# Kernel optimization log

Measured on AMD Instinct MI355X. Metric: run time of the kernel, lower is better.

## Reference

```python
import jax, jax.numpy as jnp
import numpy as np

NUM_CLASSES = 81
THRESHOLD = 0.5
NEGPOS_RATIO = 3
VARIANCE = (0.1, 0.2)


def point_form(p):
    # center-size -> corner form
    return jnp.concatenate([p[:, :2] - p[:, 2:] / 2, p[:, :2] + p[:, 2:] / 2], axis=1)


def jaccard(box_a, box_b):
    # box_a: [O,4] corners, box_b: [P,4] corners -> IoU [O,P]
    lt = jnp.maximum(box_a[:, None, :2], box_b[None, :, :2])
    rb = jnp.minimum(box_a[:, None, 2:], box_b[None, :, 2:])
    wh = jnp.clip(rb - lt, 0.0)
    inter = wh[..., 0] * wh[..., 1]
    area_a = ((box_a[:, 2] - box_a[:, 0]) * (box_a[:, 3] - box_a[:, 1]))[:, None]
    area_b = ((box_b[:, 2] - box_b[:, 0]) * (box_b[:, 3] - box_b[:, 1]))[None, :]
    return inter / (area_a + area_b - inter)


def encode(matched, priors, variances):
    # matched: [P,4] corner GT, priors: [P,4] center-size
    g_cxcy = (matched[:, :2] + matched[:, 2:]) / 2 - priors[:, :2]
    g_cxcy = g_cxcy / (variances[0] * priors[:, 2:])
    g_wh = (matched[:, 2:] - matched[:, :2]) / priors[:, 2:]
    g_wh = jnp.log(g_wh) / variances[1]
    return jnp.concatenate([g_cxcy, g_wh], axis=1)


def match_one(truths, labels, priors):
    overlaps = jaccard(truths, point_form(priors))   # [O,P]
    best_prior_idx = jnp.argmax(overlaps, axis=1)     # [O] best prior per truth
    best_truth_overlap = jnp.max(overlaps, axis=0)    # [P]
    best_truth_idx = jnp.argmax(overlaps, axis=0)     # [P] best truth per prior
    # force each truth's best prior to match that truth
    best_truth_overlap = best_truth_overlap.at[best_prior_idx].set(2.0)
    best_truth_idx = best_truth_idx.at[best_prior_idx].set(jnp.arange(truths.shape[0]))
    matched = truths[best_truth_idx]                  # [P,4]
    conf = labels[best_truth_idx].astype(jnp.int32) + 1
    conf = jnp.where(best_truth_overlap < THRESHOLD, 0, conf)
    loc = encode(matched, priors, VARIANCE)
    return loc, conf


def _loss(loc_data, conf_data, targets, priors):
    B, P, C = conf_data.shape
    loc_t, conf_t = jax.vmap(lambda t: match_one(t[:, :4], t[:, 4], priors))(targets)
    pos = conf_t > 0                                  # [B,P]
    # smooth-L1 (beta=1) over positive priors, sum reduction
    d = loc_data - loc_t
    sl1 = jnp.where(jnp.abs(d) < 1.0, 0.5 * d * d, jnp.abs(d) - 0.5)
    loss_l = jnp.sum(jnp.where(pos[..., None], sl1, 0.0))
    # per-prior CE used both for mining ranking and the final conf loss
    ce = jax.nn.logsumexp(conf_data, axis=-1) - jnp.take_along_axis(
        conf_data, conf_t[..., None], axis=-1)[..., 0]   # [B,P]
    # hard negative mining: zero positives, double argsort for rank
    loss_c_rank = jnp.where(pos, 0.0, ce)
    loss_idx = jnp.argsort(-loss_c_rank, axis=1)
    idx_rank = jnp.argsort(loss_idx, axis=1)
    num_pos = jnp.sum(pos, axis=1, keepdims=True)     # [B,1]
    num_neg = jnp.minimum(NEGPOS_RATIO * num_pos, P - 1)
    neg = idx_rank < num_neg
    sel = pos | neg
    loss_c = jnp.sum(jnp.where(sel, ce, 0.0))
    N = jnp.sum(num_pos).astype(loc_data.dtype)
    return loss_l / N, loss_c / N


def setup_inputs():
    key = jax.random.key(0)
    kl, kc, kb1, kb2, kll, kp1, kp2 = jax.random.split(key, 7)
    B, P, O, C = 64, 8732, 50, NUM_CLASSES
    loc_data = jax.random.normal(kl, (B, P, 4), jnp.float32)
    conf_data = jax.random.normal(kc, (B, P, C), jnp.float32)
    # valid GT boxes in corner form inside [0,1]
    cxcy = jax.random.uniform(kb1, (B, O, 2), minval=0.2, maxval=0.8)
    wh = jax.random.uniform(kb2, (B, O, 2), minval=0.05, maxval=0.3)
    boxes = jnp.concatenate([cxcy - wh / 2, cxcy + wh / 2], axis=-1)
    labels = jax.random.randint(kll, (B, O), 0, C - 1).astype(jnp.float32)
    targets = jnp.concatenate([boxes, labels[..., None]], axis=-1)  # [B,O,5]
    # priors in center-size form
    pcxcy = jax.random.uniform(kp1, (P, 2), minval=0.05, maxval=0.95)
    pwh = jax.random.uniform(kp2, (P, 2), minval=0.05, maxval=0.5)
    priors = jnp.concatenate([pcxcy, pwh], axis=-1)
    return {"loc_data": loc_data, "conf_data": conf_data, "targets": targets, "priors": priors}


def reference(loc_data, conf_data, targets, priors):
    return _loss(loc_data, conf_data, targets, priors)
```

## Files before the change

kernel.cpp:

```cpp
#include <hip/hip_runtime.h>
#include <float.h>

#pragma clang fp contract(off)

typedef unsigned long long ull;
typedef unsigned int u32;

#define THRESH 0.5f
#define PPT 4
#define SEL_T 512
#define ENC_SEG 1024
#define LSE_ROWS 128


__device__ __forceinline__ float sl1(float d) {
    float a = fabsf(d);
    return (a < 1.f) ? 0.5f * d * d : a - 0.5f;
}

__device__ __forceinline__ void gload16(const void* g, void* l) {
    __builtin_amdgcn_global_load_lds(
        (const __attribute__((address_space(1))) void*)g,
        (__attribute__((address_space(3))) void*)l, 16, 0, 0);
}
__device__ __forceinline__ void gload4(const void* g, void* l) {
    __builtin_amdgcn_global_load_lds(
        (const __attribute__((address_space(1))) void*)g,
        (__attribute__((address_space(3))) void*)l, 4, 0, 0);
}

__global__ __launch_bounds__(256) void k_lse(
        const float* __restrict__ conf, float* __restrict__ lse,
        u32* __restrict__ zws, int nz, long long BP) {
    __shared__ float s[LSE_ROWS * 81];
    const int bid = blockIdx.x;
    if (bid == 0)
        for (int i = threadIdx.x; i < nz; i += 256) zws[i] = 0;
    const long long r0 = (long long)bid * LSE_ROWS;
    const int w = threadIdx.x >> 6;
    const int lane = threadIdx.x & 63;
    const char* gbase = (const char*)(conf + r0 * 81);

    if (r0 + LSE_ROWS <= BP) {
        for (int i = w * 10; i < w * 10 + 10; i++)
            gload16(gbase + (size_t)i * 1024 + lane * 16, (char*)s + i * 1024);
        if (w == 0) {
            gload4(gbase + 40960 + lane * 4, (char*)s + 40960);
            gload4(gbase + 41216 + lane * 4, (char*)s + 41216);
        }
        asm volatile("s_waitcnt vmcnt(0)" ::: "memory");
    } else {
        int nfl = (int)(BP - r0) * 81;
        const float* src = (const float*)gbase;
        for (int i = threadIdx.x; i < nfl; i += 256) s[i] = src[i];
    }
    __syncthreads();

    const int row = threadIdx.x >> 1;
    const int half = threadIdx.x & 1;
    if (r0 + row < BP) {
        const float* rp = s + row * 81;
        const int c0 = half * 41;
        const int cn = half ? 40 : 41;
        float sum = 0.f;
        for (int j = 0; j < cn; j++) sum += __expf(rp[c0 + j]);
        sum += __shfl_xor(sum, 1);
        if (half == 0) lse[r0 + row] = __logf(sum);
    }
}

__global__ __launch_bounds__(256) void k_spec(
        const float* __restrict__ targets, const float* __restrict__ priors,
        float* __restrict__ bto, int* __restrict__ bti, ull* __restrict__ tbest,
        int P, int O, int S, int SB, int npairs) {
    const int bid = blockIdx.x;
    __shared__ float4 tbox[128];
    __shared__ float tarea[128];
    if (bid < SB) {
        const int b = bid / S, seg = bid % S;
        const float* trow = targets + (size_t)b * O * 5;
        for (int o = threadIdx.x; o < O; o += 256) {
            float x1 = trow[o * 5 + 0], y1 = trow[o * 5 + 1];
            float x2 = trow[o * 5 + 2], y2 = trow[o * 5 + 3];
            tbox[o] = make_float4(x1, y1, x2, y2);
            tarea[o] = (x2 - x1) * (y2 - y1);
        }
        __syncthreads();
        const int p0 = seg * (256 * PPT);
        float px1[PPT], py1[PPT], px2[PPT], py2[PPT], pa[PPT];
        float bestv[PPT]; int besto[PPT]; int pidx[PPT];
#pragma unroll
        for (int j = 0; j < PPT; j++) {
            int p = p0 + (int)threadIdx.x + j * 256;
            pidx[j] = p; bestv[j] = -1.f; besto[j] = 0;
            if (p < P) {
                float4 pr = ((const float4*)priors)[p];
                px1[j] = pr.x - pr.z / 2.f;
                py1[j] = pr.y - pr.w / 2.f;
                px2[j] = pr.x + pr.z / 2.f;
                py2[j] = pr.y + pr.w / 2.f;
                pa[j] = (px2[j] - px1[j]) * (py2[j] - py1[j]);
            } else {
                px1[j] = 2.f; py1[j] = 2.f; px2[j] = 2.f; py2[j] = 2.f; pa[j] = 1.f;
            }
        }
        for (int o = 0; o < O; o++) {
            float4 t = tbox[o];
            float ta = tarea[o];
#pragma unroll
            for (int j = 0; j < PPT; j++) {
                float lx = fmaxf(t.x, px1[j]), ly = fmaxf(t.y, py1[j]);
                float rx = fminf(t.z, px2[j]), ry = fminf(t.w, py2[j]);
                float wx = fmaxf(rx - lx, 0.f), wy = fmaxf(ry - ly, 0.f);
                float inter = wx * wy;
                float iou = 0.f;
                if (inter > 0.f) iou = inter / (ta + pa[j] - inter);
                if (iou > bestv[j]) { bestv[j] = iou; besto[j] = o; }
            }
        }
#pragma unroll
        for (int j = 0; j < PPT; j++) {
            if (pidx[j] < P) {
                bto[(size_t)b * P + pidx[j]] = bestv[j];
                bti[(size_t)b * P + pidx[j]] = besto[j];
            }
        }
    } else {
        int g = (bid - SB) * 4 + ((int)threadIdx.x >> 6);
        int lane = threadIdx.x & 63;
        if (g >= npairs) return;
        int OP = (O + 1) >> 1;
        int b = g / OP;
        int o0 = (g % OP) * 2;
        const float* trow = targets + ((size_t)b * O + o0) * 5;
        float ax1 = trow[0], ay1 = trow[1], ax2 = trow[2], ay2 = trow[3];
        float ta0 = (ax2 - ax1) * (ay2 - ay1);
        bool has1 = (o0 + 1) < O;
        float cx1 = 0, cy1 = 0, cx2 = 0, cy2 = 0, ta1 = 1.f;
        if (has1) {
            cx1 = trow[5]; cy1 = trow[6]; cx2 = trow[7]; cy2 = trow[8];
            ta1 = (cx2 - cx1) * (cy2 - cy1);
        }
        ull k0v = 0, k1v = 0;
        for (int p = lane; p < P; p += 64) {
            float4 pr = ((const float4*)priors)[p];
            float bx1 = pr.x - pr.z / 2.f;
            float by1 = pr.y - pr.w / 2.f;
            float bx2 = pr.x + pr.z / 2.f;
            float by2 = pr.y + pr.w / 2.f;
            float pa = (bx2 - bx1) * (by2 - by1);
            u32 np = ~(u32)p;
            {
                float lx = fmaxf(ax1, bx1), ly = fmaxf(ay1, by1);
                float rx = fminf(ax2, bx2), ry = fminf(ay2, by2);
                float wx = fmaxf(rx - lx, 0.f), wy = fmaxf(ry - ly, 0.f);
                float inter = wx * wy;
                float iou = 0.f;
                if (inter > 0.f) iou = inter / (ta0 + pa - inter);
                ull key = ((ull)__float_as_uint(iou) << 32) | np;
                if (key > k0v) k0v = key;
            }
            if (has1) {
                float lx = fmaxf(cx1, bx1), ly = fmaxf(cy1, by1);
                float rx = fminf(cx2, bx2), ry = fminf(cy2, by2);
                float wx = fmaxf(rx - lx, 0.f), wy = fmaxf(ry - ly, 0.f);
                float inter = wx * wy;
                float iou = 0.f;
                if (inter > 0.f) iou = inter / (ta1 + pa - inter);
                ull key = ((ull)__float_as_uint(iou) << 32) | np;
                if (key > k1v) k1v = key;
            }
        }
        for (int off = 32; off; off >>= 1) {
            ull a = __shfl_xor(k0v, off); if (a > k0v) k0v = a;
            ull d = __shfl_xor(k1v, off); if (d > k1v) k1v = d;
        }
        if (lane == 0) {
            tbest[(size_t)b * O + o0] = k0v;
            if (has1) tbest[(size_t)b * O + o0 + 1] = k1v;
        }
    }
}

__global__ __launch_bounds__(256) void k_encode_ce(
        const float* __restrict__ targets, const float* __restrict__ priors,
        const float* __restrict__ loc_data, const float* __restrict__ conf,
        const ull* __restrict__ tbest, const float* __restrict__ lse,
        float* __restrict__ F,
        int* __restrict__ conf_t,
        int* __restrict__ num_pos, float* __restrict__ loss_l,
        int P, int O) {
    const int b = blockIdx.y, seg = blockIdx.x;
    __shared__ float tr[64 * 5];
    __shared__ int ov[ENC_SEG];
    __shared__ float redf[4]; __shared__ int redi[4];
    const int p0 = seg * ENC_SEG;
    const int p1 = min(p0 + ENC_SEG, P);
    const int nprior = p1 - p0;
    const float* trow = targets + (size_t)b * O * 5;
    for (int i = threadIdx.x; i < O * 5; i += 256) tr[i] = trow[i];
    for (int i = threadIdx.x; i < nprior; i += 256) ov[i] = -1;
    __syncthreads();
    if ((int)threadIdx.x < O) {
        ull tb = tbest[(size_t)b * O + threadIdx.x];
        u32 p = ~(u32)(tb & 0xFFFFFFFFULL);
        if (p >= (u32)P) p = 0;
        if ((int)p >= p0 && (int)p < p1) atomicMax(&ov[p - p0], (int)threadIdx.x);
    }
    __syncthreads();
    float ll = 0.f; int cnt = 0;
    for (int p = p0 + (int)threadIdx.x; p < p1; p += 256) {
        size_t idx = (size_t)b * P + p;
        int o = conf_t[idx];
        int ovv = ov[p - p0];
        bool forced = ovv >= 0;
        if (forced) o = ovv;
        float ovl = F[idx];
        int cv = (!forced && ovl < THRESH) ? 0 : ((int)tr[o * 5 + 4] + 1);
        conf_t[idx] = cv;
        if (cv > 0) {
            cnt++;
            float4 pr = ((const float4*)priors)[p];
            float mx1 = tr[o * 5], my1 = tr[o * 5 + 1];
            float mx2 = tr[o * 5 + 2], my2 = tr[o * 5 + 3];
            float gx = ((mx1 + mx2) / 2.f - pr.x) / (0.1f * pr.z);
            float gy = ((my1 + my2) / 2.f - pr.y) / (0.1f * pr.w);
            float gw = logf((mx2 - mx1) / pr.z) / 0.2f;
            float gh = logf((my2 - my1) / pr.w) / 0.2f;
            float4 ld = ((const float4*)loc_data)[idx];
            ll += sl1(ld.x - gx) + sl1(ld.y - gy) + sl1(ld.z - gw) + sl1(ld.w - gh);
        }
        float tv = conf[idx * 81 + cv];
        F[idx] = lse[idx] - tv;
    }
    for (int off = 32; off; off >>= 1) {
        ll += __shfl_down(ll, off);
        cnt += __shfl_down(cnt, off);
    }
    int w = threadIdx.x >> 6;
    if ((threadIdx.x & 63) == 0) { redf[w] = ll; redi[w] = cnt; }
    __syncthreads();
    if (threadIdx.x == 0) {
        float l = 0; int c = 0;
        for (int i = 0; i < 4; i++) { l += redf[i]; c += redi[i]; }
        if (c) atomicAdd(&num_pos[b], c);
        atomicAdd(&loss_l[b], l);
    }
}

__global__ __launch_bounds__(SEL_T) void k_select(
        const float* __restrict__ ce, const int* __restrict__ conf_t,
        const int* __restrict__ num_pos, const float* __restrict__ loss_l,
        float* __restrict__ acc, u32* __restrict__ ticket,
        float* __restrict__ out, int P, int B) {
    extern __shared__ u32 sk[];
    __shared__ u32 whist[SEL_T / 64][16];
    __shared__ u32 hist[16];
    __shared__ float redf[SEL_T / 64]; __shared__ u32 redu[SEL_T / 64];
    __shared__ u32 sh_pval; __shared__ int sh_rem;
    const int b = blockIdx.x;
    const size_t base = (size_t)b * P;
    const int lane = threadIdx.x & 63;
    const int w = threadIdx.x >> 6;
    const int NW = SEL_T / 64;

    float ps = 0.f;
    for (int p = threadIdx.x; p < P; p += SEL_T) {
        int c = conf_t[base + p];
        float v = ce[base + p];
        u32 key;
        if (c > 0) { ps += v; key = 0u; }
        else key = __float_as_uint(fmaxf(v, 0.f));
        sk[p] = key;
    }
    for (int off = 32; off; off >>= 1) ps += __shfl_down(ps, off);
    if (lane == 0) redf[w] = ps;
    __syncthreads();
    float pos_sum = 0.f;
    if (threadIdx.x == 0) {
        for (int i = 0; i < NW; i++) pos_sum += redf[i];
    }

    const int np = num_pos[b];
    const int k = min(3 * np, P - 1);
    u32 pval = 0, pmask = 0; int rem = k;
    if (k > 0) {
        for (int shift = 28; shift >= 0; shift -= 4) {
            __syncthreads();
            ull a0 = 0, a1 = 0;
            for (int p = threadIdx.x; p < P; p += SEL_T) {
                u32 key = sk[p];
                if ((key & pmask) == pval) {
                    u32 dig = (key >> shift) & 15u;
                    ull inc = 1ull << ((dig & 7u) * 8u);
                    if (dig < 8u) a0 += inc; else a1 += inc;
                }
            }
            const ull M = 0x00FF00FF00FF00FFull;
            ull e0 = a0 & M, e1 = (a0 >> 8) & M, e2 = a1 & M, e3 = (a1 >> 8) & M;
            for (int off = 32; off; off >>= 1) {
                e0 += __shfl_xor(e0, off);
                e1 += __shfl_xor(e1, off);
                e2 += __shfl_xor(e2, off);
                e3 += __shfl_xor(e3, off);
            }
            if (lane == 0) {
#pragma unroll
                for (int j = 0; j < 4; j++) {
                    whist[w][2 * j]     = (u32)((e0 >> (16 * j)) & 0xFFFF);
                    whist[w][2 * j + 1] = (u32)((e1 >> (16 * j)) & 0xFFFF);
                    whist[w][8 + 2 * j]     = (u32)((e2 >> (16 * j)) & 0xFFFF);
                    whist[w][8 + 2 * j + 1] = (u32)((e3 >> (16 * j)) & 0xFFFF);
                }
            }
            __syncthreads();
            if (threadIdx.x < 16) {
                u32 h = 0;
                for (int i = 0; i < NW; i++) h += whist[i][threadIdx.x];
                hist[threadIdx.x] = h;
            }
            __syncthreads();
            if (threadIdx.x == 0) {
                u32 accu = 0; int d = 15;
                for (; d > 0; d--) {
                    u32 h = hist[d];
                    if (accu + h >= (u32)rem) break;
                    accu += h;
                }
                sh_pval = pval | ((u32)d << shift);
                sh_rem = rem - (int)accu;
            }
            __syncthreads();
            pval = sh_pval; rem = sh_rem; pmask |= (0xFu << shift);
        }
    }

    float sgt = 0.f; u32 cgt = 0;
    if (k > 0) {
        for (int p = threadIdx.x; p < P; p += SEL_T) {
            u32 key = sk[p];
            if (key > pval) { sgt += __uint_as_float(key); cgt++; }
        }
    }
    for (int off = 32; off; off >>= 1) {
        sgt += __shfl_down(sgt, off);
        cgt += __shfl_down(cgt, off);
    }
    __syncthreads();
    if (lane == 0) { redf[w] = sgt; redu[w] = cgt; }
    __syncthreads();
    if (threadIdx.x == 0) {
        float s = 0.f; u32 c = 0;
        for (int i = 0; i < NW; i++) { s += redf[i]; c += redu[i]; }
        float t = __uint_as_float(pval);
        float lc_b = pos_sum + ((k > 0) ? (s + (float)(k - (int)c) * t) : 0.f);
        atomicAdd(&acc[0], (float)np);
        atomicAdd(&acc[1], loss_l[b]);
        atomicAdd(&acc[2], lc_b);
        __threadfence();
        u32 tk = atomicAdd(ticket, 1u);
        if (tk == (u32)(B - 1)) {
            float n  = atomicAdd(&acc[0], 0.f);
            float ll = atomicAdd(&acc[1], 0.f);
            float lc = atomicAdd(&acc[2], 0.f);
            out[0] = ll / n;
            out[1] = lc / n;
        }
    }
}


extern "C" void kernel_launch(void* const* d_in, const int* in_sizes, int n_in,
                              void* d_out, int out_size, void* d_ws, size_t ws_size,
                              hipStream_t stream) {
    const float* loc     = (const float*)d_in[0];
    const float* conf    = (const float*)d_in[1];
    const float* targets = (const float*)d_in[2];
    const float* priors  = (const float*)d_in[3];

    const int P = in_sizes[3] / 4;
    const int B = in_sizes[0] / (P * 4);
    const int O = in_sizes[2] / (B * 5);
    const long long BP = (long long)B * P;

    char* ws = (char*)d_ws;
    size_t off = 0;
    int*   num_pos = (int*)(ws + off);   off += (size_t)B * sizeof(int);
    float* loss_l  = (float*)(ws + off); off += (size_t)B * sizeof(float);
    float* acc     = (float*)(ws + off); off += 4 * sizeof(float);
    u32*   ticket  = (u32*)(ws + off);   off += sizeof(u32);
    const int zwords = (int)(off >> 2);
    off = (off + 7) & ~(size_t)7;
    ull*   tbest   = (ull*)(ws + off);   off += (size_t)B * O * sizeof(ull);
    float* F       = (float*)(ws + off); off += (size_t)BP * sizeof(float);
    int*   I       = (int*)(ws + off);   off += (size_t)BP * sizeof(int);
    float* L       = (float*)(ws + off); off += (size_t)BP * sizeof(float);

    const int CB = (int)((BP + LSE_ROWS - 1) / LSE_ROWS);
    k_lse<<<CB, 256, 0, stream>>>(conf, L, (u32*)ws, zwords, BP);

    const int SEG = 256 * PPT;
    const int S = (P + SEG - 1) / SEG;
    const int SB = S * B;
    const int npairs = B * ((O + 1) / 2);
    const int TB = (npairs + 3) / 4;
    k_spec<<<SB + TB, 256, 0, stream>>>(targets, priors, F, I, tbest, P, O, S, SB, npairs);

    const int S2 = (P + ENC_SEG - 1) / ENC_SEG;
    k_encode_ce<<<dim3(S2, B), 256, 0, stream>>>(targets, priors, loc, conf, tbest, L,
                                                 F, I, num_pos, loss_l, P, O);

    k_select<<<B, SEL_T, (size_t)P * sizeof(u32), stream>>>(F, I, num_pos, loss_l,
                                                            acc, ticket, (float*)d_out, P, B);
}
```

Baseline: 373.4 us.

## Merge log-sum-exp and matching kernels into one interleaved launch

Combines the memory-bound log-sum-exp kernel and the compute-bound IoU matching kernel into a single launch. Matching blocks are spread evenly among the LSE blocks using a Bresenham-style index split, so both kinds of work share the GPU at the same time. This removes one kernel launch and the idle tail between the two launches, and lets ALU-heavy and bandwidth-heavy blocks overlap. In exchange, the merged kernel has to size its shared memory for the larger LSE tile, which may lower occupancy for the matching blocks.

```diff
diff --git a/kernel.cpp b/kernel.cpp
--- a/kernel.cpp
+++ b/kernel.cpp
@@ -29,55 +29,63 @@
         (__attribute__((address_space(3))) void*)l, 4, 0, 0);
 }
 
-__global__ __launch_bounds__(256) void k_lse(
-        const float* __restrict__ conf, float* __restrict__ lse,
-        u32* __restrict__ zws, int nz, long long BP) {
-    __shared__ float s[LSE_ROWS * 81];
+__global__ __launch_bounds__(256) void k_prep(
+        const float* __restrict__ targets, const float* __restrict__ priors,
+        const float* __restrict__ conf,
+        float* __restrict__ bto, int* __restrict__ bti, ull* __restrict__ tbest,
+        float* __restrict__ lse,
+        u32* __restrict__ zws, int nz,
+        int P, int O, int S, int SB, int SPEC, int G, int npairs, long long BP) {
+    __shared__ __align__(16) float smem[LSE_ROWS * 81];
     const int bid = blockIdx.x;
     if (bid == 0)
         for (int i = threadIdx.x; i < nz; i += 256) zws[i] = 0;
-    const long long r0 = (long long)bid * LSE_ROWS;
-    const int w = threadIdx.x >> 6;
-    const int lane = threadIdx.x & 63;
-    const char* gbase = (const char*)(conf + r0 * 81);
-
-    if (r0 + LSE_ROWS <= BP) {
-        for (int i = w * 10; i < w * 10 + 10; i++)
-            gload16(gbase + (size_t)i * 1024 + lane * 16, (char*)s + i * 1024);
-        if (w == 0) {
-            gload4(gbase + 40960 + lane * 4, (char*)s + 40960);
-            gload4(gbase + 41216 + lane * 4, (char*)s + 41216);
-        }
-        asm volatile("s_waitcnt vmcnt(0)" ::: "memory");
-    } else {
-        int nfl = (int)(BP - r0) * 81;
-        const float* src = (const float*)gbase;
-        for (int i = threadIdx.x; i < nfl; i += 256) s[i] = src[i];
-    }
-    __syncthreads();
-
-    const int row = threadIdx.x >> 1;
-    const int half = threadIdx.x & 1;
-    if (r0 + row < BP) {
-        const float* rp = s + row * 81;
-        const int c0 = half * 41;
-        const int cn = half ? 40 : 41;
-        float sum = 0.f;
-        for (int j = 0; j < cn; j++) sum += __expf(rp[c0 + j]);
-        sum += __shfl_xor(sum, 1);
-        if (half == 0) lse[r0 + row] = __logf(sum);
-    }
-}
-
-__global__ __launch_bounds__(256) void k_spec(
-        const float* __restrict__ targets, const float* __restrict__ priors,
-        float* __restrict__ bto, int* __restrict__ bti, ull* __restrict__ tbest,
-        int P, int O, int S, int SB, int npairs) {
-    const int bid = blockIdx.x;
-    __shared__ float4 tbox[128];
-    __shared__ float tarea[128];
-    if (bid < SB) {
-        const int b = bid / S, seg = bid % S;
+
+    long long t0 = (long long)bid * SPEC;
+    int k0 = (int)(t0 / G);
+    bool is_spec = (int)((t0 + SPEC) / G) > k0;
+
+    if (!is_spec) {
+        const int lb = bid - k0;
+        const long long r0 = (long long)lb * LSE_ROWS;
+        const int w = threadIdx.x >> 6;
+        const int lane = threadIdx.x & 63;
+        const char* gbase = (const char*)(conf + r0 * 81);
+
+        if (r0 + LSE_ROWS <= BP) {
+            for (int i = w * 10; i < w * 10 + 10; i++)
+                gload16(gbase + (size_t)i * 1024 + lane * 16, (char*)smem + i * 1024);
+            if (w == 0) {
+                gload4(gbase + 40960 + lane * 4, (char*)smem + 40960);
+                gload4(gbase + 41216 + lane * 4, (char*)smem + 41216);
+            }
+            asm volatile("s_waitcnt vmcnt(0)" ::: "memory");
+        } else {
+            int nfl = (int)(BP - r0) * 81;
+            const float* src = (const float*)gbase;
+            for (int i = threadIdx.x; i < nfl; i += 256) smem[i] = src[i];
+        }
+        __syncthreads();
+
+        const int row = threadIdx.x >> 1;
+        const int half = threadIdx.x & 1;
+        if (r0 + row < BP) {
+            const float* rp = smem + row * 81;
+            const int c0 = half * 41;
+            const int cn = half ? 40 : 41;
+            float sum = 0.f;
+            for (int j = 0; j < cn; j++) sum += __expf(rp[c0 + j]);
+            sum += __shfl_xor(sum, 1);
+            if (half == 0) lse[r0 + row] = __logf(sum);
+        }
+        return;
+    }
+
+    const int sidx = k0;
+    if (sidx < SB) {
+        float4* tbox = (float4*)smem;
+        float*  tarea = smem + 512;
+        const int b = sidx / S, seg = sidx % S;
         const float* trow = targets + (size_t)b * O * 5;
         for (int o = threadIdx.x; o < O; o += 256) {
             float x1 = trow[o * 5 + 0], y1 = trow[o * 5 + 1];
@@ -126,7 +134,7 @@
             }
         }
     } else {
-        int g = (bid - SB) * 4 + ((int)threadIdx.x >> 6);
+        int g = (sidx - SB) * 4 + ((int)threadIdx.x >> 6);
         int lane = threadIdx.x & 63;
         if (g >= npairs) return;
         int OP = (O + 1) >> 1;
@@ -396,15 +404,16 @@
     int*   I       = (int*)(ws + off);   off += (size_t)BP * sizeof(int);
     float* L       = (float*)(ws + off); off += (size_t)BP * sizeof(float);
 
-    const int CB = (int)((BP + LSE_ROWS - 1) / LSE_ROWS);
-    k_lse<<<CB, 256, 0, stream>>>(conf, L, (u32*)ws, zwords, BP);
-
     const int SEG = 256 * PPT;
     const int S = (P + SEG - 1) / SEG;
     const int SB = S * B;
     const int npairs = B * ((O + 1) / 2);
     const int TB = (npairs + 3) / 4;
-    k_spec<<<SB + TB, 256, 0, stream>>>(targets, priors, F, I, tbest, P, O, S, SB, npairs);
+    const int CB = (int)((BP + LSE_ROWS - 1) / LSE_ROWS);
+    const int SPEC = SB + TB;
+    const int G = CB + SPEC;
+    k_prep<<<G, 256, 0, stream>>>(targets, priors, conf, F, I, tbest, L,
+                                  (u32*)ws, zwords, P, O, S, SB, SPEC, G, npairs, BP);
 
     const int S2 = (P + ENC_SEG - 1) / ENC_SEG;
     k_encode_ce<<<dim3(S2, B), 256, 0, stream>>>(targets, priors, loc, conf, tbest, L,
```

New measurement: 359.7 us. -3.7%, faster.
